# Kernel tuning notes

Measured on AMD Instinct MI355X. Metric: run time of the kernel, lower is better.

The kernel has to match this reference:

```python
import jax, jax.numpy as jnp
import numpy as np

B, H, W, C, G = 4, 64, 64, 512, 32
EPS = 1e-5


def group_norm(x, gamma, beta):
    b, h, w, c = x.shape
    xg = x.reshape(b, h, w, G, c // G)
    mean = xg.mean(axis=(1, 2, 4), keepdims=True)
    var = xg.var(axis=(1, 2, 4), keepdims=True)
    xn = ((xg - mean) * jax.lax.rsqrt(var + EPS)).reshape(b, h, w, c)
    return xn * gamma + beta


def setup_inputs() -> dict:
    key = jax.random.key(0)
    ks = jax.random.split(key, 6)
    s = 0.02  # conv-weight init scale
    return {
        "x": jax.random.normal(ks[0], (B, H, W, C), jnp.float32),
        "gamma": jnp.ones((C,), jnp.float32),
        "beta": jnp.zeros((C,), jnp.float32),
        "Wq": jax.random.normal(ks[1], (C, C), jnp.float32) * s,
        "bq": jnp.zeros((C,), jnp.float32),
        "Wk": jax.random.normal(ks[2], (C, C), jnp.float32) * s,
        "bk": jnp.zeros((C,), jnp.float32),
        "Wv": jax.random.normal(ks[3], (C, C), jnp.float32) * s,
        "bv": jnp.zeros((C,), jnp.float32),
        "Wp": jax.random.normal(ks[4], (C, C), jnp.float32) * s,
        "bp": jnp.zeros((C,), jnp.float32),
    }


def reference(x, gamma, beta, Wq, bq, Wk, bk, Wv, bv, Wp, bp):
    b, h, w, c = x.shape
    xn = group_norm(x, gamma, beta)
    # 1x1 convs == per-pixel linear
    q = (jnp.einsum('bhwc,cd->bhwd', xn, Wq) + bq).reshape(b, h * w, c)
    k = (jnp.einsum('bhwc,cd->bhwd', xn, Wk) + bk).reshape(b, h * w, c)
    v = (jnp.einsum('bhwc,cd->bhwd', xn, Wv) + bv).reshape(b, h * w, c)
    scale = 1.0 / jnp.sqrt(jnp.asarray(c, x.dtype))
    scores = jnp.einsum('bqc,bkc->bqk', q, k) * scale  # [b, hw, hw]
    attn = jax.nn.softmax(scores, axis=-1)
    out = jnp.einsum('bqk,bkc->bqc', attn, v).reshape(b, h, w, c)
    return jnp.einsum('bhwc,cd->bhwd', out, Wp) + bp + x
```

## Files before the change

kernel.cpp:

```cpp
#include <hip/hip_runtime.h>

typedef unsigned short u16;
typedef unsigned char u8;
typedef float f32x4 __attribute__((ext_vector_type(4)));
typedef int i32x8 __attribute__((ext_vector_type(8)));

#define CH 512
#define HW 4096
#define TOKENS 16384
#define NGRP 32

__device__ __forceinline__ u8 f2fp8(float f) {
  return (u8)(__builtin_amdgcn_cvt_pk_fp8_f32(f, f, 0, false) & 0xff);
}
__device__ __forceinline__ unsigned f2fp8x4(float a, float b, float c, float d) {
  int lo = __builtin_amdgcn_cvt_pk_fp8_f32(a, b, 0, false);
  return (unsigned)__builtin_amdgcn_cvt_pk_fp8_f32(c, d, lo, true);
}
__device__ __forceinline__ unsigned nib4(float x) {
  float a = fabsf(x) * 4.0f;
  unsigned c = (unsigned)(a >= 0.25f) + (a >= 0.75f) + (a >= 1.25f) + (a >= 1.75f) +
               (a >= 2.5f) + (a >= 3.5f) + (a >= 5.0f);
  return c | ((__float_as_uint(x) >> 28) & 8u);
}
__device__ __forceinline__ u16 pk4(float a, float b, float c, float d) {
  return (u16)(nib4(a) | (nib4(b) << 4) | (nib4(c) << 8) | (nib4(d) << 12));
}

#define GLOAD16(gp, lp)                                                        \
  __builtin_amdgcn_global_load_lds(                                            \
      (const __attribute__((address_space(1))) unsigned int*)(const void*)(gp),\
      (__attribute__((address_space(3))) unsigned int*)(void*)(lp), 16, 0, 0)

#define RD8(dst, buf, row) do {                                                \
    int base_ = (row) * 128, sw_ = ((row) & 7) << 4;                           \
    uint4 lo_ = *(const uint4*)(&buf[base_ + ((h * 32) ^ sw_)]);               \
    uint4 hi_ = *(const uint4*)(&buf[base_ + ((h * 32 + 16) ^ sw_)]);          \
    dst[0] = (int)lo_.x; dst[1] = (int)lo_.y; dst[2] = (int)lo_.z;             \
    dst[3] = (int)lo_.w; dst[4] = (int)hi_.x; dst[5] = (int)hi_.y;             \
    dst[6] = (int)hi_.z; dst[7] = (int)hi_.w;                                  \
  } while (0)

__global__ void gn_stats(const float* __restrict__ x, float2* __restrict__ stats) {
  int bg = blockIdx.x;
  int b = bg >> 5, g = bg & 31;
  const float* base = x + (size_t)b * HW * CH + g * 16;
  float s = 0.f, s2 = 0.f;
  for (int p = threadIdx.x; p < HW; p += 256) {
    const float4* row = (const float4*)(base + (size_t)p * CH);
#pragma unroll
    for (int q = 0; q < 4; ++q) {
      float4 v = row[q];
      s += v.x + v.y + v.z + v.w;
      s2 += v.x * v.x + v.y * v.y + v.z * v.z + v.w * v.w;
    }
  }
#pragma unroll
  for (int o = 32; o; o >>= 1) { s += __shfl_down(s, o); s2 += __shfl_down(s2, o); }
  __shared__ float rs[4], rs2[4];
  int wid = threadIdx.x >> 6, lane = threadIdx.x & 63;
  if (lane == 0) { rs[wid] = s; rs2[wid] = s2; }
  __syncthreads();
  if (threadIdx.x == 0) {
    float S = rs[0] + rs[1] + rs[2] + rs[3];
    float S2 = rs2[0] + rs2[1] + rs2[2] + rs2[3];
    float mean = S * (1.f / 65536.f);
    float var = S2 * (1.f / 65536.f) - mean * mean;
    stats[bg] = make_float2(mean, rsqrtf(var + 1e-5f));
  }
}

__global__ void gn_apply8(const float* __restrict__ x, const float* __restrict__ gamma,
                          const float* __restrict__ beta, const float2* __restrict__ stats,
                          u8* __restrict__ xn8) {
  size_t i = (size_t)blockIdx.x * blockDim.x + threadIdx.x;
  size_t e0 = i * 8;
  int c = (int)(e0 & (CH - 1));
  size_t t = e0 >> 9;
  int b = (int)(t >> 12);
  float2 st = stats[b * NGRP + (c >> 4)];
  float4 v0 = *(const float4*)(x + t * CH + c);
  float4 v1 = *(const float4*)(x + t * CH + c + 4);
  float4 g0 = *(const float4*)(gamma + c);
  float4 g1 = *(const float4*)(gamma + c + 4);
  float4 b0 = *(const float4*)(beta + c);
  float4 b1 = *(const float4*)(beta + c + 4);
  float o[8];
  o[0] = (v0.x - st.x) * st.y * g0.x + b0.x;
  o[1] = (v0.y - st.x) * st.y * g0.y + b0.y;
  o[2] = (v0.z - st.x) * st.y * g0.z + b0.z;
  o[3] = (v0.w - st.x) * st.y * g0.w + b0.w;
  o[4] = (v1.x - st.x) * st.y * g1.x + b1.x;
  o[5] = (v1.y - st.x) * st.y * g1.y + b1.y;
  o[6] = (v1.z - st.x) * st.y * g1.z + b1.z;
  o[7] = (v1.w - st.x) * st.y * g1.w + b1.w;
  uint2 pk;
  pk.x = f2fp8x4(o[0], o[1], o[2], o[3]);
  pk.y = f2fp8x4(o[4], o[5], o[6], o[7]);
  *(uint2*)(xn8 + e0) = pk;
}

__global__ void transpose_w8(const float* __restrict__ W0, const float* __restrict__ W1,
                             const float* __restrict__ W2, const float* __restrict__ W3,
                             u8* __restrict__ T0, u8* __restrict__ T1,
                             u8* __restrict__ T2, u8* __restrict__ T3) {
  const float* W; u8* T;
  switch (blockIdx.z) {
    case 0: W = W0; T = T0; break;
    case 1: W = W1; T = T1; break;
    case 2: W = W2; T = T2; break;
    default: W = W3; T = T3; break;
  }
  __shared__ float tile[32][33];
  int tx = threadIdx.x, ty = threadIdx.y;
  int x0 = blockIdx.x * 32, y0 = blockIdx.y * 32;
#pragma unroll
  for (int r = 0; r < 32; r += 8) tile[ty + r][tx] = W[(size_t)(y0 + ty + r) * CH + x0 + tx];
  __syncthreads();
#pragma unroll
  for (int r = 0; r < 32; r += 8) T[(size_t)(x0 + ty + r) * CH + y0 + tx] = f2fp8(tile[tx][ty + r]);
}

__global__ __launch_bounds__(256) void qkvmx(const u8* __restrict__ A,
                                             const u8* __restrict__ Bt,
                                             const float* __restrict__ bq,
                                             const float* __restrict__ bk,
                                             const float* __restrict__ bv,
                                             u8* __restrict__ Q4, u8* __restrict__ K4,
                                             u8* __restrict__ V4) {
  constexpr int BK = 128;
  const int K = CH;
  __shared__ __align__(16) u8 lA[128 * BK];
  __shared__ __align__(16) u8 lB[128 * BK];
  const int bm = blockIdx.y * 128, bn = blockIdx.x * 128;
  const int tid = threadIdx.x, lane = tid & 63, wid = tid >> 6;
  const int wm = (wid >> 1) * 64, wn = (wid & 1) * 64;
  const int r0 = lane & 15, h = lane >> 4;

  const int srow = lane >> 3;
  const int scol = ((lane & 7) * 16) ^ ((srow & 7) << 4);
  size_t aoff[4], boff[4];
#pragma unroll
  for (int s = 0; s < 4; ++s) {
    int row = wid * 32 + s * 8 + srow;
    aoff[s] = (size_t)(bm + row) * K + scol;
    boff[s] = (size_t)(bn + row) * K + scol;
  }

  f32x4 acc[4][4] = {};
  for (int kt = 0; kt < K; kt += BK) {
    __syncthreads();
#pragma unroll
    for (int s = 0; s < 4; ++s) {
      GLOAD16(A + aoff[s] + kt, &lA[(wid * 4 + s) * 1024]);
      GLOAD16(Bt + boff[s] + kt, &lB[(wid * 4 + s) * 1024]);
    }
    __syncthreads();
    i32x8 bf[4];
#pragma unroll
    for (int j = 0; j < 4; ++j) RD8(bf[j], lB, wn + j * 16 + r0);
#pragma unroll
    for (int i = 0; i < 4; ++i) {
      i32x8 af;
      RD8(af, lA, wm + i * 16 + r0);
#pragma unroll
      for (int j = 0; j < 4; ++j)
        acc[i][j] = __builtin_amdgcn_mfma_scale_f32_16x16x128_f8f6f4(
            af, bf[j], acc[i][j], 0, 0, 0, 127, 0, 127);
    }
  }

  const int chn = (bn + wn) >> 9;
  const int nb = (bn + wn) & 511;
  if (chn == 2) {
#pragma unroll
    for (int j = 0; j < 4; ++j) {
      int nn = nb + j * 16 + r0;
      float bvv = bv[nn];
#pragma unroll
      for (int i = 0; i < 4; ++i) {
        int m0 = bm + wm + i * 16 + h * 4;
        int bb = m0 >> 12, tl = m0 & (HW - 1);
        *(u16*)(V4 + ((size_t)bb * CH + nn) * (HW / 2) + (tl >> 1)) =
            pk4(acc[i][j][0] + bvv, acc[i][j][1] + bvv,
                acc[i][j][2] + bvv, acc[i][j][3] + bvv);
      }
    }
  } else {
    u8* P4 = chn == 0 ? Q4 : K4;
    const float* bb_ = chn == 0 ? bq : bk;
    float bj[4];
#pragma unroll
    for (int j = 0; j < 4; ++j) bj[j] = bb_[nb + j * 16 + r0];
#pragma unroll
    for (int i = 0; i < 4; ++i) {
#pragma unroll
      for (int r = 0; r < 4; ++r) {
        int m0r = bm + wm + i * 16 + h * 4 + r;
        *(u16*)(P4 + (size_t)m0r * 256 + (nb >> 1) + 2 * r0) =
            pk4(acc[i][0][r] + bj[0], acc[i][1][r] + bj[1],
                acc[i][2][r] + bj[2], acc[i][3][r] + bj[3]);
      }
    }
  }
}

__global__ __launch_bounds__(512, 2) void flash64(const u8* __restrict__ Q4,
                                                  const u8* __restrict__ K4,
                                                  const u8* __restrict__ V4,
                                                  u8* __restrict__ O8, float scl) {
  __shared__ __align__(16) u8 QL[64 * 256];
  __shared__ __align__(16) u8 PL[64 * 128];
  __shared__ float RSW[8 * 64];

  const int p = blockIdx.x;
  const int g = (p & 7) * 32 + (p >> 3);
  const int z = g >> 6, qt = g & 63;
  const int bm = qt * 64;
  const u8* Q = Q4 + (size_t)z * HW * 256;
  const u8* K = K4 + (size_t)z * HW * 256;
  const u8* V = V4 + (size_t)z * CH * (HW / 2);
  u8* O = O8 + (size_t)z * HW * CH;

  const int tid = threadIdx.x, lane = tid & 63, w = tid >> 6;
  const int r0 = lane & 15, h = lane >> 4;

  {
    int row = tid >> 3, c0 = (tid & 7) * 32;
    uint4 a = *(const uint4*)(Q + (size_t)(bm + row) * 256 + c0);
    uint4 b = *(const uint4*)(Q + (size_t)(bm + row) * 256 + c0 + 16);
    int sw = (row & 3) << 4;
    *(uint4*)&QL[row * 256 + (c0 ^ sw)] = a;
    *(uint4*)&QL[row * 256 + ((c0 + 16) ^ sw)] = b;
  }
  __syncthreads();

  f32x4 oacc[4][4] = {};
  f32x4 rsum[4] = {};

  for (int it = 0; it < 32; ++it) {
    const int k0 = it * 128;
    f32x4 sacc[4] = {};
#pragma unroll
    for (int ks = 0; ks < 4; ++ks) {
      i32x8 bf;
      {
        uint4 t = *(const uint4*)(K + (size_t)(k0 + w * 16 + r0) * 256 + ks * 64 + h * 16);
        bf[0] = (int)t.x; bf[1] = (int)t.y; bf[2] = (int)t.z; bf[3] = (int)t.w;
        bf[4] = 0; bf[5] = 0; bf[6] = 0; bf[7] = 0;
      }
#pragma unroll
      for (int i = 0; i < 4; ++i) {
        int qr = i * 16 + r0;
        uint4 t = *(const uint4*)&QL[qr * 256 + ((ks * 64 + h * 16) ^ ((qr & 3) << 4))];
        i32x8 af;
        af[0] = (int)t.x; af[1] = (int)t.y; af[2] = (int)t.z; af[3] = (int)t.w;
        af[4] = 0; af[5] = 0; af[6] = 0; af[7] = 0;
        sacc[i] = __builtin_amdgcn_mfma_scale_f32_16x16x128_f8f6f4(
            af, bf, sacc[i], 4, 4, 0, 125, 0, 125);
      }
    }
    __syncthreads();
#pragma unroll
    for (int i = 0; i < 4; ++i)
#pragma unroll
      for (int r = 0; r < 4; ++r) {
        float e = __expf(sacc[i][r] * scl);
        rsum[i][r] += e;
        int qr = i * 16 + h * 4 + r;
        PL[qr * 128 + ((w * 16 + r0) ^ (((qr >> 2) & 3) << 4))] = f2fp8(e);
      }
    __syncthreads();
#pragma unroll
    for (int i = 0; i < 4; ++i) {
      int qr = i * 16 + r0;
      int sw = ((qr >> 2) & 3) << 4;
      uint4 lo = *(const uint4*)&PL[qr * 128 + ((h * 32) ^ sw)];
      uint4 hi = *(const uint4*)&PL[qr * 128 + ((h * 32 + 16) ^ sw)];
      i32x8 af;
      af[0] = (int)lo.x; af[1] = (int)lo.y; af[2] = (int)lo.z; af[3] = (int)lo.w;
      af[4] = (int)hi.x; af[5] = (int)hi.y; af[6] = (int)hi.z; af[7] = (int)hi.w;
#pragma unroll
      for (int j = 0; j < 4; ++j) {
        uint4 t = *(const uint4*)(V + (size_t)(w * 64 + j * 16 + r0) * (HW / 2) +
                                  it * 64 + h * 16);
        i32x8 bf;
        bf[0] = (int)t.x; bf[1] = (int)t.y; bf[2] = (int)t.z; bf[3] = (int)t.w;
        bf[4] = 0; bf[5] = 0; bf[6] = 0; bf[7] = 0;
        oacc[i][j] = __builtin_amdgcn_mfma_scale_f32_16x16x128_f8f6f4(
            af, bf, oacc[i][j], 0, 4, 0, 127, 0, 125);
      }
    }
  }

#pragma unroll
  for (int i = 0; i < 4; ++i)
#pragma unroll
    for (int r = 0; r < 4; ++r) {
      float v = rsum[i][r];
#pragma unroll
      for (int m = 1; m < 16; m <<= 1) v += __shfl_xor(v, m);
      if (r0 == 0) RSW[w * 64 + i * 16 + h * 4 + r] = v;
    }
  __syncthreads();

#pragma unroll
  for (int i = 0; i < 4; ++i)
#pragma unroll
    for (int r = 0; r < 4; ++r) {
      int qr = i * 16 + h * 4 + r;
      float tot = 0.f;
#pragma unroll
      for (int ww = 0; ww < 8; ++ww) tot += RSW[ww * 64 + qr];
      float inv = 1.0f / tot;
      u8* dst = O + (size_t)(bm + qr) * CH + w * 64;
#pragma unroll
      for (int j = 0; j < 4; ++j)
        dst[j * 16 + r0] = f2fp8(oacc[i][j][r] * inv);
    }
}

__global__ __launch_bounds__(256) void projmx(const u8* __restrict__ A,
                                              const u8* __restrict__ Bt,
                                              const float* __restrict__ bias,
                                              const float* __restrict__ residual,
                                              float* __restrict__ Cout) {
  constexpr int BK = 128;
  const int K = CH, N = CH;
  __shared__ __align__(16) u8 lA[128 * BK];
  __shared__ __align__(16) u8 lB[128 * BK];
  const int bm = blockIdx.y * 128, bn = blockIdx.x * 128;
  const int tid = threadIdx.x, lane = tid & 63, wid = tid >> 6;
  const int wm = (wid >> 1) * 64, wn = (wid & 1) * 64;
  const int r0 = lane & 15, h = lane >> 4;

  const int srow = lane >> 3;
  const int scol = ((lane & 7) * 16) ^ ((srow & 7) << 4);
  size_t aoff[4], boff[4];
#pragma unroll
  for (int s = 0; s < 4; ++s) {
    int row = wid * 32 + s * 8 + srow;
    aoff[s] = (size_t)(bm + row) * K + scol;
    boff[s] = (size_t)(bn + row) * K + scol;
  }

  f32x4 acc[4][4] = {};
  for (int kt = 0; kt < K; kt += BK) {
    __syncthreads();
#pragma unroll
    for (int s = 0; s < 4; ++s) {
      GLOAD16(A + aoff[s] + kt, &lA[(wid * 4 + s) * 1024]);
      GLOAD16(Bt + boff[s] + kt, &lB[(wid * 4 + s) * 1024]);
    }
    __syncthreads();
    i32x8 bf[4];
#pragma unroll
    for (int j = 0; j < 4; ++j) RD8(bf[j], lB, wn + j * 16 + r0);
#pragma unroll
    for (int i = 0; i < 4; ++i) {
      i32x8 af;
      RD8(af, lA, wm + i * 16 + r0);
#pragma unroll
      for (int j = 0; j < 4; ++j)
        acc[i][j] = __builtin_amdgcn_mfma_scale_f32_16x16x128_f8f6f4(
            af, bf[j], acc[i][j], 0, 0, 0, 127, 0, 127);
    }
  }

#pragma unroll
  for (int j = 0; j < 4; ++j) {
    int n = bn + wn + j * 16 + r0;
    float bvv = bias[n];
#pragma unroll
    for (int i = 0; i < 4; ++i) {
      int m0 = bm + wm + i * 16 + h * 4;
#pragma unroll
      for (int r = 0; r < 4; ++r) {
        size_t idx = (size_t)(m0 + r) * N + n;
        Cout[idx] = acc[i][j][r] + bvv + residual[idx];
      }
    }
  }
}

extern "C" void kernel_launch(void* const* d_in, const int* in_sizes, int n_in,
                              void* d_out, int out_size, void* d_ws, size_t ws_size,
                              hipStream_t stream) {
  (void)in_sizes; (void)n_in; (void)out_size; (void)ws_size;
  const float* x     = (const float*)d_in[0];
  const float* gamma = (const float*)d_in[1];
  const float* beta  = (const float*)d_in[2];
  const float* Wq    = (const float*)d_in[3];
  const float* bq    = (const float*)d_in[4];
  const float* Wk    = (const float*)d_in[5];
  const float* bk    = (const float*)d_in[6];
  const float* Wv    = (const float*)d_in[7];
  const float* bv    = (const float*)d_in[8];
  const float* Wp    = (const float*)d_in[9];
  const float* bp    = (const float*)d_in[10];
  float* out = (float*)d_out;

  char* ws = (char*)d_ws;
  size_t off = 0;
  auto alloc = [&](size_t bytes) -> void* {
    void* p = ws + off;
    off += (bytes + 255) & ~(size_t)255;
    return p;
  };
  const size_t X8 = (size_t)TOKENS * CH;
  const size_t X4 = (size_t)TOKENS * CH / 2;
  const size_t W8 = (size_t)CH * CH;

  float2* stats = (float2*)alloc(128 * sizeof(float2));
  u8* xn8   = (u8*)alloc(X8);
  u8* O8    = (u8*)alloc(X8);
  u8* Q4    = (u8*)alloc(X4);
  u8* K4    = (u8*)alloc(X4);
  u8* V4    = (u8*)alloc(X4);
  u8* Wqkv8 = (u8*)alloc(3 * W8);
  u8* Wp8   = (u8*)alloc(W8);

  gn_stats<<<128, 256, 0, stream>>>(x, stats);
  gn_apply8<<<TOKENS * CH / 8 / 256, 256, 0, stream>>>(x, gamma, beta, stats, xn8);
  transpose_w8<<<dim3(16, 16, 4), dim3(32, 8), 0, stream>>>(
      Wq, Wk, Wv, Wp, Wqkv8, Wqkv8 + (size_t)CH * CH, Wqkv8 + 2 * (size_t)CH * CH, Wp8);

  qkvmx<<<dim3(1536 / 128, TOKENS / 128), 256, 0, stream>>>(
      xn8, Wqkv8, bq, bk, bv, Q4, K4, V4);

  const float scl = 0.044194173824159216f;
  flash64<<<dim3(256), 512, 0, stream>>>(Q4, K4, V4, O8, scl);

  projmx<<<dim3(4, TOKENS / 128), 256, 0, stream>>>(O8, Wp8, bp, x, out);
}
```

Baseline: 177.0 us.

## Halve flash attention query tile to 32 rows and double block count

The attention kernel now processes 32 query rows per block instead of 64, launching 512 blocks rather than 256 so the grid better fills the GPU's compute units. The QK^T MFMA operands are swapped so K is the A operand, which lets P be written to LDS as packed 32-bit words instead of single bytes, with a new swizzle. Row-sum reduction is simplified and normalization factors are computed once per block. The cost is that each block now streams the full K and V for only half as many queries, doubling global K/V traffic per query.

```diff
diff --git a/kernel.cpp b/kernel.cpp
--- a/kernel.cpp
+++ b/kernel.cpp
@@ -205,18 +205,18 @@
   }
 }
 
-__global__ __launch_bounds__(512, 2) void flash64(const u8* __restrict__ Q4,
+__global__ __launch_bounds__(512, 2) void flash32(const u8* __restrict__ Q4,
                                                   const u8* __restrict__ K4,
                                                   const u8* __restrict__ V4,
                                                   u8* __restrict__ O8, float scl) {
-  __shared__ __align__(16) u8 QL[64 * 256];
-  __shared__ __align__(16) u8 PL[64 * 128];
-  __shared__ float RSW[8 * 64];
+  __shared__ __align__(16) u8 QL[32 * 256];
+  __shared__ __align__(16) u8 PL[32 * 128];
+  __shared__ float RSW[8 * 32];
 
   const int p = blockIdx.x;
-  const int g = (p & 7) * 32 + (p >> 3);
-  const int z = g >> 6, qt = g & 63;
-  const int bm = qt * 64;
+  const int g = (p & 7) * 64 + (p >> 3);
+  const int z = g >> 7, qt = g & 127;
+  const int bm = qt * 32;
   const u8* Q = Q4 + (size_t)z * HW * 256;
   const u8* K = K4 + (size_t)z * HW * 256;
   const u8* V = V4 + (size_t)z * CH * (HW / 2);
@@ -226,57 +226,56 @@
   const int r0 = lane & 15, h = lane >> 4;
 
   {
-    int row = tid >> 3, c0 = (tid & 7) * 32;
+    int row = tid >> 4, c0 = (tid & 15) * 16;
     uint4 a = *(const uint4*)(Q + (size_t)(bm + row) * 256 + c0);
-    uint4 b = *(const uint4*)(Q + (size_t)(bm + row) * 256 + c0 + 16);
-    int sw = (row & 3) << 4;
-    *(uint4*)&QL[row * 256 + (c0 ^ sw)] = a;
-    *(uint4*)&QL[row * 256 + ((c0 + 16) ^ sw)] = b;
+    *(uint4*)&QL[row * 256 + (c0 ^ ((row & 7) << 4))] = a;
   }
   __syncthreads();
 
-  f32x4 oacc[4][4] = {};
-  f32x4 rsum[4] = {};
+  f32x4 oacc[2][4] = {};
+  float rsum[2] = {0.f, 0.f};
 
   for (int it = 0; it < 32; ++it) {
     const int k0 = it * 128;
-    f32x4 sacc[4] = {};
+    f32x4 sacc[2] = {};
 #pragma unroll
     for (int ks = 0; ks < 4; ++ks) {
-      i32x8 bf;
+      i32x8 af;
       {
         uint4 t = *(const uint4*)(K + (size_t)(k0 + w * 16 + r0) * 256 + ks * 64 + h * 16);
+        af[0] = (int)t.x; af[1] = (int)t.y; af[2] = (int)t.z; af[3] = (int)t.w;
+        af[4] = 0; af[5] = 0; af[6] = 0; af[7] = 0;
+      }
+#pragma unroll
+      for (int j = 0; j < 2; ++j) {
+        uint4 t = *(const uint4*)&QL[(j * 16 + r0) * 256 +
+                                     ((ks * 64 + h * 16) ^ ((r0 & 7) << 4))];
+        i32x8 bf;
         bf[0] = (int)t.x; bf[1] = (int)t.y; bf[2] = (int)t.z; bf[3] = (int)t.w;
         bf[4] = 0; bf[5] = 0; bf[6] = 0; bf[7] = 0;
-      }
-#pragma unroll
-      for (int i = 0; i < 4; ++i) {
-        int qr = i * 16 + r0;
-        uint4 t = *(const uint4*)&QL[qr * 256 + ((ks * 64 + h * 16) ^ ((qr & 3) << 4))];
-        i32x8 af;
-        af[0] = (int)t.x; af[1] = (int)t.y; af[2] = (int)t.z; af[3] = (int)t.w;
-        af[4] = 0; af[5] = 0; af[6] = 0; af[7] = 0;
-        sacc[i] = __builtin_amdgcn_mfma_scale_f32_16x16x128_f8f6f4(
-            af, bf, sacc[i], 4, 4, 0, 125, 0, 125);
-      }
-    }
-    __syncthreads();
-#pragma unroll
-    for (int i = 0; i < 4; ++i)
-#pragma unroll
-      for (int r = 0; r < 4; ++r) {
-        float e = __expf(sacc[i][r] * scl);
-        rsum[i][r] += e;
-        int qr = i * 16 + h * 4 + r;
-        PL[qr * 128 + ((w * 16 + r0) ^ (((qr >> 2) & 3) << 4))] = f2fp8(e);
-      }
-    __syncthreads();
-#pragma unroll
-    for (int i = 0; i < 4; ++i) {
-      int qr = i * 16 + r0;
-      int sw = ((qr >> 2) & 3) << 4;
-      uint4 lo = *(const uint4*)&PL[qr * 128 + ((h * 32) ^ sw)];
-      uint4 hi = *(const uint4*)&PL[qr * 128 + ((h * 32 + 16) ^ sw)];
+        sacc[j] = __builtin_amdgcn_mfma_scale_f32_16x16x128_f8f6f4(
+            af, bf, sacc[j], 4, 4, 0, 125, 0, 125);
+      }
+    }
+    __syncthreads();
+#pragma unroll
+    for (int j = 0; j < 2; ++j) {
+      float e0 = __expf(sacc[j][0] * scl);
+      float e1 = __expf(sacc[j][1] * scl);
+      float e2 = __expf(sacc[j][2] * scl);
+      float e3 = __expf(sacc[j][3] * scl);
+      rsum[j] += e0 + e1 + e2 + e3;
+      unsigned pw = (unsigned)f2fp8(e0) | ((unsigned)f2fp8(e1) << 8) |
+                    ((unsigned)f2fp8(e2) << 16) | ((unsigned)f2fp8(e3) << 24);
+      *(unsigned*)&PL[(j * 16 + r0) * 128 + (((w * 16) ^ ((r0 & 7) << 4)) + h * 4)] = pw;
+    }
+    __syncthreads();
+#pragma unroll
+    for (int i = 0; i < 2; ++i) {
+      int q = i * 16 + r0;
+      int sw = (r0 & 7) << 4;
+      uint4 lo = *(const uint4*)&PL[q * 128 + ((h * 32) ^ sw)];
+      uint4 hi = *(const uint4*)&PL[q * 128 + ((h * 32 + 16) ^ sw)];
       i32x8 af;
       af[0] = (int)lo.x; af[1] = (int)lo.y; af[2] = (int)lo.z; af[3] = (int)lo.w;
       af[4] = (int)hi.x; af[5] = (int)hi.y; af[6] = (int)hi.z; af[7] = (int)hi.w;
@@ -294,26 +293,28 @@
   }
 
 #pragma unroll
-  for (int i = 0; i < 4; ++i)
+  for (int j = 0; j < 2; ++j) {
+    float v = rsum[j];
+    v += __shfl_xor(v, 16);
+    v += __shfl_xor(v, 32);
+    if (h == 0) RSW[w * 32 + j * 16 + r0] = v;
+  }
+  __syncthreads();
+  if (tid < 32) {
+    float tot = 0.f;
+#pragma unroll
+    for (int ww = 0; ww < 8; ++ww) tot += RSW[ww * 32 + tid];
+    RSW[tid] = 1.0f / tot;
+  }
+  __syncthreads();
+
+#pragma unroll
+  for (int i = 0; i < 2; ++i)
 #pragma unroll
     for (int r = 0; r < 4; ++r) {
-      float v = rsum[i][r];
-#pragma unroll
-      for (int m = 1; m < 16; m <<= 1) v += __shfl_xor(v, m);
-      if (r0 == 0) RSW[w * 64 + i * 16 + h * 4 + r] = v;
-    }
-  __syncthreads();
-
-#pragma unroll
-  for (int i = 0; i < 4; ++i)
-#pragma unroll
-    for (int r = 0; r < 4; ++r) {
-      int qr = i * 16 + h * 4 + r;
-      float tot = 0.f;
-#pragma unroll
-      for (int ww = 0; ww < 8; ++ww) tot += RSW[ww * 64 + qr];
-      float inv = 1.0f / tot;
-      u8* dst = O + (size_t)(bm + qr) * CH + w * 64;
+      int q = i * 16 + h * 4 + r;
+      float inv = RSW[q];
+      u8* dst = O + (size_t)(bm + q) * CH + w * 64;
 #pragma unroll
       for (int j = 0; j < 4; ++j)
         dst[j * 16 + r0] = f2fp8(oacc[i][j][r] * inv);
@@ -429,7 +430,7 @@
       xn8, Wqkv8, bq, bk, bv, Q4, K4, V4);
 
   const float scl = 0.044194173824159216f;
-  flash64<<<dim3(256), 512, 0, stream>>>(Q4, K4, V4, O8, scl);
+  flash32<<<dim3(512), 512, 0, stream>>>(Q4, K4, V4, O8, scl);
 
   projmx<<<dim3(4, TOKENS / 128), 256, 0, stream>>>(O8, Wp8, bp, x, out);
 }
```

Result: slower. 187.4 us (+5.9%).
